# Optimization experiments

Measured on AMD Instinct MI355X. Metric: run time of the kernel, lower is better.

The kernel has to match this reference:

```python
import jax, jax.numpy as jnp
import numpy as np

C = 128          # multiplicity of 0e and 1o irreps
N = 16384        # number of tokens / points
SQRT2 = 2.0 ** 0.5
SQRT3 = 3.0 ** 0.5


def _tensor_square(s, v):
    """Per-channel symmetric tensor square of (1x0e + 1x1o).
    s: (N,C) scalars, v: (N,C,3) vectors.
    Returns ss:(N,C) 0e, sv:(N,C,3) 1o, vv0:(N,C) 0e, q:(N,C,5) 2e."""
    ss = s * s
    sv = SQRT2 * s[..., None] * v
    vv0 = jnp.sum(v * v, axis=-1) / SQRT3
    x, y, z = v[..., 0], v[..., 1], v[..., 2]
    q = jnp.stack([
        SQRT3 * x * y,
        SQRT3 * y * z,
        (2.0 * z * z - x * x - y * y) / 2.0,
        SQRT3 * x * z,
        SQRT3 * (x * x - y * y) / 2.0,
    ], axis=-1)
    return ss, sv, vv0, q


def _block(s, v, w1, w2, w0, wv):
    """_SelfInteractionBlock: tensor_square + concat/regroup + invariant-gated MLP + equivariant Linear."""
    ss, sv, vv0, q = _tensor_square(s, v)
    # regrouped features: 3C x 0e, 2C x 1o, C x 2e
    sc = jnp.concatenate([s, ss, vv0], axis=-1)            # (N, 3C)
    vec = jnp.concatenate([v, sv], axis=1)                 # (N, 2C, 3)
    # gate MLP on invariants (fan-in normalized, silu hidden)
    h = jax.nn.silu(sc @ w1 / jnp.sqrt(jnp.float32(sc.shape[-1])))
    g = h @ w2 / jnp.sqrt(jnp.float32(h.shape[-1]))        # (N, 6C) one gate per irrep
    g_s = g[:, :3 * C]
    g_v = g[:, 3 * C:5 * C]
    # (2e gates multiply q, which is dropped by the Linear to Cx0e+Cx1o)
    sc = sc * g_s
    vec = vec * g_v[..., None]
    # block-diagonal equivariant Linear -> C x 0e + C x 1o
    out_s = sc @ w0 / jnp.sqrt(jnp.float32(sc.shape[-1]))                      # (N, C)
    out_v = jnp.einsum('nmd,mc->ncd', vec, wv) / jnp.sqrt(jnp.float32(vec.shape[1]))  # (N, C, 3)
    return out_s, out_v


def _eq_layernorm(s, v, g0, g1, eps=1e-6):
    mu = jnp.mean(s, axis=-1, keepdims=True)
    sd = jnp.sqrt(jnp.mean((s - mu) ** 2, axis=-1, keepdims=True) + eps)
    s = (s - mu) / sd * g0
    rms = jnp.sqrt(jnp.mean(v * v, axis=(1, 2), keepdims=True) + eps)
    v = v / rms * g1[None, :, None]
    return s, v


def setup_inputs() -> dict:
    key = jax.random.key(0)
    ks = jax.random.split(key, 6)
    x = jax.random.normal(ks[0], (N, 4 * C), dtype=jnp.float32)
    mlp_w1 = jax.random.normal(ks[1], (2, 3 * C, 3 * C), dtype=jnp.float32)
    mlp_w2 = jax.random.normal(ks[2], (2, 3 * C, 6 * C), dtype=jnp.float32)
    lin_w0 = jax.random.normal(ks[3], (2, 3 * C, C), dtype=jnp.float32)
    lin_w1 = jax.random.normal(ks[4], (2, 2 * C, C), dtype=jnp.float32)
    ln_g0 = jnp.ones((C,), dtype=jnp.float32)
    ln_g1 = jnp.ones((C,), dtype=jnp.float32)
    return {"x": x, "mlp_w1": mlp_w1, "mlp_w2": mlp_w2,
            "lin_w0": lin_w0, "lin_w1": lin_w1, "ln_g0": ln_g0, "ln_g1": ln_g1}


def reference(x, mlp_w1, mlp_w2, lin_w0, lin_w1, ln_g0, ln_g1):
    n = x.shape[0]
    s = x[:, :C]                         # C x 0e
    v = x[:, C:].reshape(n, C, 3)        # C x 1o
    n_layers = mlp_w1.shape[0]
    for i in range(n_layers):
        ds, dv = _block(s, v, mlp_w1[i], mlp_w2[i], lin_w0[i], lin_w1[i])
        s = s + ds   # residual
        v = v + dv
        if i != n_layers - 1:  # norm on all but last layer (norm_last=False)
            s, v = _eq_layernorm(s, v, ln_g0, ln_g1)
    return jnp.concatenate([s, v.reshape(n, 3 * C)], axis=-1)
```

## Files before the change

### kernel.cpp

```cpp
#include <hip/hip_runtime.h>


typedef _Float16 half8 __attribute__((ext_vector_type(8)));
typedef float floatx4 __attribute__((ext_vector_type(4)));

static inline int cdiv_h(int a, int b){ return (a + b - 1) / b; }


__device__ __forceinline__ void stage16(const char* gaddr, char* lds_wave_base){
  __builtin_amdgcn_global_load_lds((const __attribute__((address_space(1))) unsigned int*)gaddr,
                                   (__attribute__((address_space(3))) unsigned int*)lds_wave_base,
                                   16, 0, 0);
}

__device__ __forceinline__ float wave_sum64(float x){
  #pragma unroll
  for (int m = 32; m; m >>= 1) x += __shfl_xor(x, m, 64);
  return x;
}

__device__ __forceinline__ void split_store(_Float16* p0, _Float16* p1, float v){
  _Float16 hi = (_Float16)v;
  *p0 = hi;
  *p1 = (_Float16)(v - (float)hi);
}

__global__ __launch_bounds__(256) void prep_all(const float* __restrict__ w1,
                                                const float* __restrict__ w2,
                                                const float* __restrict__ w0,
                                                const float* __restrict__ wv,
                                                _Float16* __restrict__ W){
  const int PER_L = 475136;
  int idx = blockIdx.x*256 + threadIdx.x;
  if (idx >= 2*PER_L) return;
  int l = idx / PER_L;
  int r = idx - l*PER_L;
  const float RS384 = 0.051031036307982884f;
  _Float16* WL = W + (size_t)l*1425408;
  const float* src; _Float16* dst; int K, ldw, col, k; float scale;
  if (r < 147456){
    src = w1 + (size_t)l*147456; dst = WL;            K = 384; ldw = 384; scale = RS384;
    col = r / 384; k = r - col*384;
  } else if (r < 393216){
    r -= 147456;
    src = w2 + (size_t)l*294912; dst = WL + 442368;   K = 384; ldw = 768; scale = RS384;
    col = r / 384; k = r - col*384;
  } else if (r < 442368){
    r -= 393216;
    src = w0 + (size_t)l*49152;  dst = WL + 1179648;  K = 384; ldw = 128; scale = RS384;
    col = r / 384; k = r - col*384;
  } else {
    r -= 442368;
    src = wv + (size_t)l*32768;  dst = WL + 1327104;  K = 256; ldw = 128; scale = 0.0625f;
    col = r / 256; k = r - col*256;
  }
  float v = src[(size_t)k*ldw + col] * scale;
  _Float16 hi = (_Float16)v;
  _Float16 lo = (_Float16)(v - (float)hi);
  size_t b = (size_t)col*3*K + k;
  dst[b]       = hi;
  dst[b + K]   = lo;
  dst[b + 2*K] = hi;
}

__global__ __launch_bounds__(256) void e0_fused(const float* __restrict__ x,
                                                float* __restrict__ S,
                                                float* __restrict__ V,
                                                _Float16* __restrict__ A1,
                                                int row0){
  __shared__ alignas(16) float lx[4][512];
  const int n0 = blockIdx.x*4;
  const int tid = threadIdx.x;
  const float4* xs = (const float4*)(x + (size_t)(row0 + n0)*512);
  float4* ls = (float4*)(&lx[0][0]);
  ls[tid]       = xs[tid];
  ls[tid + 256] = xs[tid + 256];
  __syncthreads();
  const int w = tid >> 6, lane = tid & 63;
  const int n = n0 + w;
  const float* row = &lx[w][0];
  #pragma unroll
  for (int h = 0; h < 2; ++h){
    int ch = h*64 + lane;
    float s = row[ch];
    S[(size_t)n*128 + ch] = s;
    float vv = 0.f;
    #pragma unroll
    for (int d = 0; d < 3; ++d){
      float vd = row[128 + ch*3 + d];
      V[((size_t)n*3 + d)*128 + ch] = vd;
      vv += vd*vd;
    }
    float vals[3] = { s, s*s, vv * 0.5773502691896258f };
    #pragma unroll
    for (int q = 0; q < 3; ++q){
      size_t b = (size_t)n*768 + q*128 + ch;
      split_store(&A1[b], &A1[b + 384], vals[q]);
    }
  }
}

__global__ __launch_bounds__(256) void e3_fin(float* __restrict__ S, float* __restrict__ V,
                                              const float* __restrict__ OS, const float* __restrict__ OV,
                                              const float* __restrict__ g0, const float* __restrict__ g1,
                                              float* __restrict__ out, _Float16* __restrict__ A1,
                                              int row0, int doln){
  int n = blockIdx.x*4 + (threadIdx.x >> 6);
  int lane = threadIdx.x & 63;
  size_t sb = (size_t)n*128;
  size_t vb = (size_t)n*384;
  float s0 = S[sb + lane]      + OS[sb + lane];
  float s1 = S[sb + 64 + lane] + OS[sb + 64 + lane];
  float v[6];
  #pragma unroll
  for (int k = 0; k < 6; ++k) v[k] = V[vb + k*64 + lane] + OV[vb + k*64 + lane];

  if (doln){
    float mu = wave_sum64(s0 + s1) * (1.0f/128.0f);
    float d0 = s0 - mu, d1 = s1 - mu;
    float var = wave_sum64(d0*d0 + d1*d1) * (1.0f/128.0f);
    float sd = sqrtf(var + 1e-6f);
    float vvsum = 0.f;
    #pragma unroll
    for (int k = 0; k < 6; ++k) vvsum += v[k]*v[k];
    float rms = sqrtf(wave_sum64(vvsum) * (1.0f/384.0f) + 1e-6f);
    float s0n = d0 / sd * g0[lane];
    float s1n = d1 / sd * g0[64 + lane];
    S[sb + lane]      = s0n;
    S[sb + 64 + lane] = s1n;
    float vn[6];
    #pragma unroll
    for (int k = 0; k < 6; ++k){
      int j = k*64 + lane;
      vn[k] = v[k] / rms * g1[j & 127];
      V[vb + j] = vn[k];
    }
    float vv_a = vn[0]*vn[0] + vn[2]*vn[2] + vn[4]*vn[4];
    float vv_b = vn[1]*vn[1] + vn[3]*vn[3] + vn[5]*vn[5];
    float va[3] = { s0n, s0n*s0n, vv_a * 0.5773502691896258f };
    float vbv[3]= { s1n, s1n*s1n, vv_b * 0.5773502691896258f };
    #pragma unroll
    for (int q = 0; q < 3; ++q){
      size_t ba = (size_t)n*768 + q*128 + lane;
      split_store(&A1[ba], &A1[ba + 384], va[q]);
      size_t bb = ba + 64;
      split_store(&A1[bb], &A1[bb + 384], vbv[q]);
    }
  } else {
    size_t ob = (size_t)(row0 + n)*512;
    out[ob + lane]      = s0;
    out[ob + 64 + lane] = s1;
    #pragma unroll
    for (int k = 0; k < 6; ++k){
      int j = k*64 + lane;
      int d = j >> 7, ch = j & 127;
      out[ob + 128 + ch*3 + d] = v[k];
    }
  }
}

__device__ __forceinline__ void gemm_mainloop(const _Float16* __restrict__ A,
                                              const _Float16* __restrict__ BT,
                                              int lda, int kbase, int m0, int c0,
                                              _Float16 (&lA)[2][4096],
                                              _Float16 (&lB)[2][4096],
                                              floatx4 (&acc)[4][4]){
  const int nsc  = kbase >> 5;
  const int nch  = 3*nsc;
  const int ldbt = 3*kbase;
  const int tid  = threadIdx.x;
  const int wave = tid >> 6, lane = tid & 63;
  const int wm = wave & 1, wn = wave >> 1;
  const int r = lane & 15, kg = lane >> 4;
  const int slot = kg ^ ((r >> 1) & 3);

  auto stage = [&](int c, int buf){
    const int ka = ((c < nsc) ? c : c - nsc) << 5;
    const int kb = c << 5;
    #pragma unroll
    for (int p = 0; p < 2; ++p){
      const int lbase = wave*1024 + p*4096;
      const int off = lbase + lane*16;
      const int row = off >> 6;
      const int bir = (off & 63) ^ (((off >> 7) & 3) << 4);
      const char* ga = (const char*)A  + (((size_t)(m0 + row))*lda  + ka)*2 + bir;
      stage16(ga, (char*)(&lA[buf][0]) + lbase);
      const char* gb = (const char*)BT + (((size_t)(c0 + row))*ldbt + kb)*2 + bir;
      stage16(gb, (char*)(&lB[buf][0]) + lbase);
    }
  };

  stage(0, 0);
  for (int c = 0; c < nch; ++c){
    __syncthreads();
    if (c + 1 < nch) stage(c + 1, (c + 1) & 1);
    const char* a_ = (const char*)&lA[c & 1][0];
    const char* b_ = (const char*)&lB[c & 1][0];
    half8 af[4], bf[4];
    #pragma unroll
    for (int mt = 0; mt < 4; ++mt)
      af[mt] = *(const half8*)(a_ + ((wm*64 + mt*16 + r)*64 + slot*16));
    #pragma unroll
    for (int nt = 0; nt < 4; ++nt)
      bf[nt] = *(const half8*)(b_ + ((wn*64 + nt*16 + r)*64 + slot*16));
    #pragma unroll
    for (int mt = 0; mt < 4; ++mt)
      #pragma unroll
      for (int nt = 0; nt < 4; ++nt)
        acc[mt][nt] = __builtin_amdgcn_mfma_f32_16x16x32_f16(af[mt], bf[nt], acc[mt][nt], 0, 0, 0);
  }
}

template<int MODE>
__global__ __launch_bounds__(256) void gemm_split(const _Float16* __restrict__ A,
                                                  const _Float16* __restrict__ BT,
                                                  float* __restrict__ C,
                                                  _Float16* __restrict__ SP,
                                                  const float* __restrict__ S,
                                                  const float* __restrict__ V,
                                                  _Float16* __restrict__ A1,
                                                  _Float16* __restrict__ A4,
                                                  int lda, int kbase, int ldc){
  __shared__ alignas(16) _Float16 lA[2][4096];
  __shared__ alignas(16) _Float16 lB[2][4096];
  const int m0 = blockIdx.x << 7, c0 = blockIdx.y << 7;
  floatx4 acc[4][4];
  #pragma unroll
  for (int i = 0; i < 4; ++i)
    #pragma unroll
    for (int j = 0; j < 4; ++j) acc[i][j] = (floatx4){0.f, 0.f, 0.f, 0.f};

  gemm_mainloop(A, BT, lda, kbase, m0, c0, lA, lB, acc);

  const int wave = threadIdx.x >> 6, lane = threadIdx.x & 63;
  const int wm = wave & 1, wn = wave >> 1;
  const int r = lane & 15, kg = lane >> 4;

  #pragma unroll
  for (int mt = 0; mt < 4; ++mt){
    #pragma unroll
    for (int nt = 0; nt < 4; ++nt){
      #pragma unroll
      for (int i = 0; i < 4; ++i){
        const int row = m0 + wm*64 + mt*16 + kg*4 + i;
        const int col = c0 + wn*64 + nt*16 + r;
        float g = acc[mt][nt][i];
        if (MODE == 0){
          C[(size_t)row*ldc + col] = g;
        } else if (MODE == 1){
          float h = g / (1.0f + __expf(-g));
          split_store(&SP[(size_t)row*768 + col], &SP[(size_t)row*768 + 384 + col], h);
        } else {
          if (c0 < 384){
            size_t b = (size_t)row*768 + col;
            float sc = (float)A1[b] + (float)A1[b + 384];
            split_store(&A1[b], &A1[b + 384], sc * g);
          } else {
            int mm = col - 384;
            int ch = mm & 127;
            float gm = g;
            if (c0 == 512) gm *= 1.4142135623730951f * S[(size_t)row*128 + ch];
            #pragma unroll
            for (int d = 0; d < 3; ++d){
              float val = V[((size_t)row*3 + d)*128 + ch] * gm;
              size_t b = ((size_t)row*3 + d)*512 + mm;
              split_store(&A4[b], &A4[b + 256], val);
            }
          }
        }
      }
    }
  }
}

__global__ __launch_bounds__(256) void gemm_pair(const _Float16* __restrict__ Aa,
                                                 const _Float16* __restrict__ Ba,
                                                 float* __restrict__ Ca, int nb0,
                                                 const _Float16* __restrict__ Ab,
                                                 const _Float16* __restrict__ Bb,
                                                 float* __restrict__ Cb){
  __shared__ alignas(16) _Float16 lA[2][4096];
  __shared__ alignas(16) _Float16 lB[2][4096];
  const _Float16 *A, *BT; float* C; int lda, kbase, m0;
  if ((int)blockIdx.x < nb0){
    A = Aa; BT = Ba; C = Ca; lda = 768; kbase = 384; m0 = (int)blockIdx.x << 7;
  } else {
    A = Ab; BT = Bb; C = Cb; lda = 512; kbase = 256; m0 = ((int)blockIdx.x - nb0) << 7;
  }
  floatx4 acc[4][4];
  #pragma unroll
  for (int i = 0; i < 4; ++i)
    #pragma unroll
    for (int j = 0; j < 4; ++j) acc[i][j] = (floatx4){0.f, 0.f, 0.f, 0.f};

  gemm_mainloop(A, BT, lda, kbase, m0, 0, lA, lB, acc);

  const int wave = threadIdx.x >> 6, lane = threadIdx.x & 63;
  const int wm = wave & 1, wn = wave >> 1;
  const int r = lane & 15, kg = lane >> 4;
  #pragma unroll
  for (int mt = 0; mt < 4; ++mt)
    #pragma unroll
    for (int nt = 0; nt < 4; ++nt)
      #pragma unroll
      for (int i = 0; i < 4; ++i){
        const int row = m0 + wm*64 + mt*16 + kg*4 + i;
        const int col = wn*64 + nt*16 + r;
        C[(size_t)row*128 + col] = acc[mt][nt][i];
      }
}


extern "C" void kernel_launch(void* const* d_in, const int* in_sizes, int n_in,
                              void* d_out, int out_size, void* d_ws, size_t ws_size,
                              hipStream_t stream){
  const float* x  = (const float*)d_in[0];
  const float* w1 = (const float*)d_in[1];
  const float* w2 = (const float*)d_in[2];
  const float* w0 = (const float*)d_in[3];
  const float* wv = (const float*)d_in[4];
  const float* g0 = (const float*)d_in[5];
  const float* g1 = (const float*)d_in[6];
  float* out = (float*)d_out;
  const int N = in_sizes[0] / 512;

  const size_t HL = 1425408;
  _Float16* W = (_Float16*)d_ws;
  const size_t wbytes = 2*HL*2;

  int cnum = 128;
  for (int cc = 1; cc <= 128; cc <<= 1){
    size_t need = wbytes + (size_t)(N/cc)*10240;
    if (need <= ws_size){ cnum = cc; break; }
  }
  const int R = N / cnum;

  char* p = (char*)d_ws + wbytes;
  float*    Sst = (float*)p;     p += (size_t)R*512;
  float*    Vst = (float*)p;     p += (size_t)R*1536;
  _Float16* A1  = (_Float16*)p;  p += (size_t)R*1536;
  _Float16* A2  = (_Float16*)p;  p += (size_t)R*1536;
  _Float16* A4  = (_Float16*)p;  p += (size_t)R*3072;
  float*    OS  = (float*)p;     p += (size_t)R*512;
  float*    OV  = (float*)p;     p += (size_t)R*1536;

  prep_all<<<cdiv_h(2*475136,256),256,0,stream>>>(w1, w2, w0, wv, W);

  for (int chk = 0; chk < cnum; ++chk){
    const int row0 = chk*R;
    e0_fused<<<R/4,256,0,stream>>>(x, Sst, Vst, A1, row0);
    for (int l = 0; l < 2; ++l){
      _Float16* W1p = W + (size_t)l*HL;
      _Float16* W2p = W1p + 442368;
      _Float16* W0p = W1p + 1179648;
      _Float16* WVp = W1p + 1327104;
      gemm_split<1><<<dim3(R/128,3),256,0,stream>>>(A1, W1p, nullptr, A2,
          nullptr, nullptr, nullptr, nullptr, 768, 384, 0);
      gemm_split<2><<<dim3(R/128,5),256,0,stream>>>(A2, W2p, nullptr, nullptr,
          Sst, Vst, A1, A4, 768, 384, 0);
      gemm_pair<<<R/32,256,0,stream>>>(A1, W0p, OS, R/128, A4, WVp, OV);
      e3_fin<<<R/4,256,0,stream>>>(Sst, Vst, OS, OV, g0, g1, out, A1, row0, (l == 0) ? 1 : 0);
    }
  }
}
```

Measured before the change: 422.6 us.

## Stage GEMM epilogues through LDS for coalesced vector stores and swap grid order

The gemm_split epilogues now write results into the reused LDS staging buffer, then emit them as coalesced 8- and 16-byte global stores. The hi/lo fp16 halves are packed together and unzipped into separate row segments, and A1/V operands are loaded into LDS cooperatively rather than through scattered per-element reads. The grid is transposed so the column-tile index varies fastest, letting blocks that share A rows run close together for cache reuse. The cost is several extra __syncthreads passes and half-wave idling during each epilogue phase.

```diff
diff --git a/kernel.cpp b/kernel.cpp
--- a/kernel.cpp
+++ b/kernel.cpp
@@ -23,6 +23,21 @@
   _Float16 hi = (_Float16)v;
   *p0 = hi;
   *p1 = (_Float16)(v - (float)hi);
+}
+
+__device__ __forceinline__ unsigned int pack_split(float v){
+  union { _Float16 h[2]; unsigned int u; } pk;
+  _Float16 hi = (_Float16)v;
+  pk.h[0] = hi;
+  pk.h[1] = (_Float16)(v - (float)hi);
+  return pk.u;
+}
+
+__device__ __forceinline__ void unzip16(uint4 p, uint2& hi, uint2& lo){
+  hi.x = (p.x & 0xffffu) | (p.y << 16);
+  hi.y = (p.z & 0xffffu) | (p.w << 16);
+  lo.x = (p.x >> 16) | (p.y & 0xffff0000u);
+  lo.y = (p.z >> 16) | (p.w & 0xffff0000u);
 }
 
 __global__ __launch_bounds__(256) void prep_all(const float* __restrict__ w1,
@@ -162,8 +177,7 @@
 __device__ __forceinline__ void gemm_mainloop(const _Float16* __restrict__ A,
                                               const _Float16* __restrict__ BT,
                                               int lda, int kbase, int m0, int c0,
-                                              _Float16 (&lA)[2][4096],
-                                              _Float16 (&lB)[2][4096],
+                                              _Float16 (&ls)[4][4096],
                                               floatx4 (&acc)[4][4]){
   const int nsc  = kbase >> 5;
   const int nch  = 3*nsc;
@@ -184,9 +198,9 @@
       const int row = off >> 6;
       const int bir = (off & 63) ^ (((off >> 7) & 3) << 4);
       const char* ga = (const char*)A  + (((size_t)(m0 + row))*lda  + ka)*2 + bir;
-      stage16(ga, (char*)(&lA[buf][0]) + lbase);
+      stage16(ga, (char*)(&ls[buf][0]) + lbase);
       const char* gb = (const char*)BT + (((size_t)(c0 + row))*ldbt + kb)*2 + bir;
-      stage16(gb, (char*)(&lB[buf][0]) + lbase);
+      stage16(gb, (char*)(&ls[2 + buf][0]) + lbase);
     }
   };
 
@@ -194,8 +208,8 @@
   for (int c = 0; c < nch; ++c){
     __syncthreads();
     if (c + 1 < nch) stage(c + 1, (c + 1) & 1);
-    const char* a_ = (const char*)&lA[c & 1][0];
-    const char* b_ = (const char*)&lB[c & 1][0];
+    const char* a_ = (const char*)&ls[c & 1][0];
+    const char* b_ = (const char*)&ls[2 + (c & 1)][0];
     half8 af[4], bf[4];
     #pragma unroll
     for (int mt = 0; mt < 4; ++mt)
@@ -214,59 +228,136 @@
 template<int MODE>
 __global__ __launch_bounds__(256) void gemm_split(const _Float16* __restrict__ A,
                                                   const _Float16* __restrict__ BT,
-                                                  float* __restrict__ C,
-                                                  _Float16* __restrict__ SP,
+                                                  _Float16* __restrict__ OUT,
                                                   const float* __restrict__ S,
                                                   const float* __restrict__ V,
-                                                  _Float16* __restrict__ A1,
+                                                  _Float16* __restrict__ A1g,
                                                   _Float16* __restrict__ A4,
-                                                  int lda, int kbase, int ldc){
-  __shared__ alignas(16) _Float16 lA[2][4096];
-  __shared__ alignas(16) _Float16 lB[2][4096];
-  const int m0 = blockIdx.x << 7, c0 = blockIdx.y << 7;
+                                                  int lda, int kbase){
+  __shared__ alignas(16) _Float16 ls[4][4096];
+  const int c0 = blockIdx.x << 7, m0 = blockIdx.y << 7;
   floatx4 acc[4][4];
   #pragma unroll
   for (int i = 0; i < 4; ++i)
     #pragma unroll
     for (int j = 0; j < 4; ++j) acc[i][j] = (floatx4){0.f, 0.f, 0.f, 0.f};
 
-  gemm_mainloop(A, BT, lda, kbase, m0, c0, lA, lB, acc);
-
-  const int wave = threadIdx.x >> 6, lane = threadIdx.x & 63;
+  gemm_mainloop(A, BT, lda, kbase, m0, c0, ls, acc);
+
+  const int tid = threadIdx.x;
+  const int wave = tid >> 6, lane = tid & 63;
   const int wm = wave & 1, wn = wave >> 1;
   const int r = lane & 15, kg = lane >> 4;
-
-  #pragma unroll
-  for (int mt = 0; mt < 4; ++mt){
-    #pragma unroll
-    for (int nt = 0; nt < 4; ++nt){
+  char* scr = (char*)&ls[0][0];
+
+  if (MODE == 1 || c0 < 384){
+    #pragma unroll
+    for (int h = 0; h < 2; ++h){
+      __syncthreads();
+      if (MODE == 2){
+        #pragma unroll
+        for (int j = 0; j < 4; ++j){
+          int lin = j*256 + tid;
+          int rl = lin >> 4, seg = lin & 15;
+          const char* gp = (const char*)(A1g + (size_t)(m0 + h*64 + rl)*768 + c0) + seg*16;
+          *(float4*)(scr + rl*256 + seg*16)         = *(const float4*)gp;
+          *(float4*)(scr + 16384 + rl*256 + seg*16) = *(const float4*)(gp + 768);
+        }
+      }
+      __syncthreads();
+      if (wm == h){
+        #pragma unroll
+        for (int mt = 0; mt < 4; ++mt)
+          #pragma unroll
+          for (int nt = 0; nt < 4; ++nt)
+            #pragma unroll
+            for (int i = 0; i < 4; ++i){
+              int rl = mt*16 + kg*4 + i;
+              int cl = wn*64 + nt*16 + r;
+              float g = acc[mt][nt][i];
+              if (MODE == 1){
+                float hh = g / (1.0f + __expf(-g));
+                ((unsigned int*)scr)[rl*128 + cl] = pack_split(hh);
+              } else {
+                _Float16* phi = (_Float16*)scr + rl*128 + cl;
+                _Float16* plo = (_Float16*)(scr + 16384) + rl*128 + cl;
+                float sc = (float)*phi + (float)*plo;
+                split_store(phi, plo, sc * g);
+              }
+            }
+      }
+      __syncthreads();
+      if (MODE == 1){
+        #pragma unroll
+        for (int j = 0; j < 8; ++j){
+          int lin = j*256 + tid;
+          int rl = lin >> 5, seg = lin & 31;
+          uint4 p = *(const uint4*)(scr + rl*512 + seg*16);
+          uint2 hi, lo; unzip16(p, hi, lo);
+          _Float16* rowp = OUT + (size_t)(m0 + h*64 + rl)*768 + c0 + seg*4;
+          *(uint2*)rowp         = hi;
+          *(uint2*)(rowp + 384) = lo;
+        }
+      } else {
+        #pragma unroll
+        for (int j = 0; j < 4; ++j){
+          int lin = j*256 + tid;
+          int rl = lin >> 4, seg = lin & 15;
+          char* gp = (char*)(A1g + (size_t)(m0 + h*64 + rl)*768 + c0) + seg*16;
+          *(float4*)gp         = *(const float4*)(scr + rl*256 + seg*16);
+          *(float4*)(gp + 768) = *(const float4*)(scr + 16384 + rl*256 + seg*16);
+        }
+      }
+    }
+  } else {
+    const int mmbase = c0 - 384;
+    if (mmbase == 128){
       #pragma unroll
-      for (int i = 0; i < 4; ++i){
-        const int row = m0 + wm*64 + mt*16 + kg*4 + i;
-        const int col = c0 + wn*64 + nt*16 + r;
-        float g = acc[mt][nt][i];
-        if (MODE == 0){
-          C[(size_t)row*ldc + col] = g;
-        } else if (MODE == 1){
-          float h = g / (1.0f + __expf(-g));
-          split_store(&SP[(size_t)row*768 + col], &SP[(size_t)row*768 + 384 + col], h);
-        } else {
-          if (c0 < 384){
-            size_t b = (size_t)row*768 + col;
-            float sc = (float)A1[b] + (float)A1[b + 384];
-            split_store(&A1[b], &A1[b + 384], sc * g);
-          } else {
-            int mm = col - 384;
-            int ch = mm & 127;
-            float gm = g;
-            if (c0 == 512) gm *= 1.4142135623730951f * S[(size_t)row*128 + ch];
+      for (int mt = 0; mt < 4; ++mt)
+        #pragma unroll
+        for (int nt = 0; nt < 4; ++nt)
+          #pragma unroll
+          for (int i = 0; i < 4; ++i){
+            int row = m0 + wm*64 + mt*16 + kg*4 + i;
+            int ch  = wn*64 + nt*16 + r;
+            acc[mt][nt][i] *= 1.4142135623730951f * S[(size_t)row*128 + ch];
+          }
+    }
+    for (int d = 0; d < 3; ++d){
+      #pragma unroll
+      for (int h = 0; h < 2; ++h){
+        __syncthreads();
+        #pragma unroll
+        for (int j = 0; j < 8; ++j){
+          int lin = j*256 + tid;
+          int rl = lin >> 5, seg = lin & 31;
+          *(float4*)(scr + rl*512 + seg*16) =
+            *(const float4*)(V + ((size_t)(m0 + h*64 + rl)*3 + d)*128 + seg*4);
+        }
+        __syncthreads();
+        if (wm == h){
+          #pragma unroll
+          for (int mt = 0; mt < 4; ++mt)
             #pragma unroll
-            for (int d = 0; d < 3; ++d){
-              float val = V[((size_t)row*3 + d)*128 + ch] * gm;
-              size_t b = ((size_t)row*3 + d)*512 + mm;
-              split_store(&A4[b], &A4[b + 256], val);
-            }
-          }
+            for (int nt = 0; nt < 4; ++nt)
+              #pragma unroll
+              for (int i = 0; i < 4; ++i){
+                int rl = mt*16 + kg*4 + i;
+                int cl = wn*64 + nt*16 + r;
+                float vv = ((const float*)scr)[rl*128 + cl];
+                ((unsigned int*)scr)[rl*128 + cl] = pack_split(vv * acc[mt][nt][i]);
+              }
+        }
+        __syncthreads();
+        #pragma unroll
+        for (int j = 0; j < 8; ++j){
+          int lin = j*256 + tid;
+          int rl = lin >> 5, seg = lin & 31;
+          uint4 p = *(const uint4*)(scr + rl*512 + seg*16);
+          uint2 hi, lo; unzip16(p, hi, lo);
+          _Float16* rowp = A4 + ((size_t)(m0 + h*64 + rl)*3 + d)*512 + mmbase + seg*4;
+          *(uint2*)rowp         = hi;
+          *(uint2*)(rowp + 256) = lo;
         }
       }
     }
@@ -279,8 +370,7 @@
                                                  const _Float16* __restrict__ Ab,
                                                  const _Float16* __restrict__ Bb,
                                                  float* __restrict__ Cb){
-  __shared__ alignas(16) _Float16 lA[2][4096];
-  __shared__ alignas(16) _Float16 lB[2][4096];
+  __shared__ alignas(16) _Float16 ls[4][4096];
   const _Float16 *A, *BT; float* C; int lda, kbase, m0;
   if ((int)blockIdx.x < nb0){
     A = Aa; BT = Ba; C = Ca; lda = 768; kbase = 384; m0 = (int)blockIdx.x << 7;
@@ -293,7 +383,7 @@
     #pragma unroll
     for (int j = 0; j < 4; ++j) acc[i][j] = (floatx4){0.f, 0.f, 0.f, 0.f};
 
-  gemm_mainloop(A, BT, lda, kbase, m0, 0, lA, lB, acc);
+  gemm_mainloop(A, BT, lda, kbase, m0, 0, ls, acc);
 
   const int wave = threadIdx.x >> 6, lane = threadIdx.x & 63;
   const int wm = wave & 1, wn = wave >> 1;
@@ -354,10 +444,10 @@
       _Float16* W2p = W1p + 442368;
       _Float16* W0p = W1p + 1179648;
       _Float16* WVp = W1p + 1327104;
-      gemm_split<1><<<dim3(R/128,3),256,0,stream>>>(A1, W1p, nullptr, A2,
-          nullptr, nullptr, nullptr, nullptr, 768, 384, 0);
-      gemm_split<2><<<dim3(R/128,5),256,0,stream>>>(A2, W2p, nullptr, nullptr,
-          Sst, Vst, A1, A4, 768, 384, 0);
+      gemm_split<1><<<dim3(3, R/128),256,0,stream>>>(A1, W1p, A2,
+          nullptr, nullptr, nullptr, nullptr, 768, 384);
+      gemm_split<2><<<dim3(5, R/128),256,0,stream>>>(A2, W2p, nullptr,
+          Sst, Vst, A1, A4, 768, 384);
       gemm_pair<<<R/32,256,0,stream>>>(A1, W0p, OS, R/128, A4, WVp, OV);
       e3_fin<<<R/4,256,0,stream>>>(Sst, Vst, OS, OV, g0, g1, out, A1, row0, (l == 0) ? 1 : 0);
     }
```

Measured after the change: 461.9 us. 1.09x slower.
